# Performance work log

Measured on AMD Instinct MI355X. Metric: run time of the kernel, lower is better.

The kernel has to match this reference:

```python
import jax, jax.numpy as jnp
import numpy as np

TOP_P_THRESHOLD = 1.0 - 0.9  # hardcoded in the original module (ignores self.top_p)

def setup_inputs() -> dict:
    key = jax.random.key(0)
    k1, _ = jax.random.split(key)
    batch, vocab = 128, 128000
    logits = jax.random.normal(k1, (batch, vocab), dtype=jnp.float32) * 3.0
    position_ids = jnp.arange(batch, dtype=jnp.int32)
    return {"logits": logits, "position_ids": position_ids}

def reference(logits, position_ids):
    # Ascending sort along vocab axis (jnp.sort default), matching original.
    sorted_logits = jnp.sort(logits, axis=-1)
    sorted_indices = jnp.argsort(logits, axis=-1)
    # Cumulative probability in ascending-logit order.
    cum_probs = jnp.cumsum(jax.nn.softmax(sorted_logits, axis=-1), axis=-1)
    keep = cum_probs > TOP_P_THRESHOLD
    # Kept sorted values; dropped positions get -inf (the fill_value).
    vals = jnp.where(keep, sorted_logits, -jnp.inf)
    # Scatter back to original vocab positions: mask[..., sorted_indices] = vals
    # is equivalent to gathering vals with the inverse permutation.
    inv_perm = jnp.argsort(sorted_indices, axis=-1)
    mask = jnp.take_along_axis(vals, inv_perm, axis=-1)
    return mask
```

## Files before the change

### kernel.cpp

```cpp
#include <hip/hip_runtime.h>
#include <stdint.h>
#include <math.h>

#define TPB 256
#define CH 16
#define LISTCAP 160
#define FIN_TPB 256
#define FB_TPB 1024
#define FB_TIE 1024
#define S_FIX 4096.0f
#define DROPV (-1.0e30f)

struct SelT { double P; double THR; uint32_t pfx; uint32_t pad; };

__device__ __forceinline__ uint32_t tokey(float f) {
  uint32_t b = __float_as_uint(f);
  return (b & 0x80000000u) ? ~b : (b | 0x80000000u);
}
__device__ __forceinline__ float fromkey(uint32_t k) {
  uint32_t b = (k & 0x80000000u) ? (k ^ 0x80000000u) : ~k;
  return __uint_as_float(b);
}
__device__ __forceinline__ float scrub(float f) {
  uint32_t b = __float_as_uint(f) & 0x7FFFFFFFu;
  if (b >= 0x7F7F0000u) return DROPV;
  return f;
}
__device__ __forceinline__ unsigned long long tofix(float u) {
  return (unsigned long long)(u * S_FIX);
}

__device__ __forceinline__ void wave_selectD(const double* __restrict__ bins, int nb,
                                             int bits, int lane,
                                             double* sP, uint32_t* sPrefix, double THR) {
  const int per = nb >> 6;
  double lsum = 0.0;
  for (int k = 0; k < per; ++k) lsum += bins[lane * per + k];
  double v = lsum;
#pragma unroll
  for (int off = 1; off < 64; off <<= 1) {
    double o = __shfl_up(v, off, 64);
    if (lane >= off) v += o;
  }
  const double excl = v - lsum;
  const double P = *sP;
  int lbin = -1;
  double lP = 0.0;
  double rr = P + excl;
  for (int k = 0; k < per; ++k) {
    double m = bins[lane * per + k];
    double nr = rr + m;
    if (lbin < 0 && nr > THR) { lbin = lane * per + k; lP = rr; }
    rr = nr;
  }
  unsigned long long got = __ballot(lbin >= 0);
  int bsel;
  double Pn;
  if (got) {
    int src = __ffsll(got) - 1;
    bsel = __shfl(lbin, src, 64);
    Pn = __shfl(lP, src, 64);
  } else {
    int hb = -1;
    double pb = P;
    rr = P + excl;
    for (int k = 0; k < per; ++k) {
      double m = bins[lane * per + k];
      if (m > 0.0) { hb = lane * per + k; pb = rr; }
      rr += m;
    }
#pragma unroll
    for (int off = 32; off; off >>= 1) {
      int ob = __shfl_xor(hb, off, 64);
      double opb = __shfl_xor(pb, off, 64);
      if (ob > hb) { hb = ob; pb = opb; }
    }
    bsel = hb < 0 ? (nb - 1) : hb;
    Pn = pb;
  }
  if (lane == 0) {
    *sPrefix = (*sPrefix << bits) | (uint32_t)bsel;
    *sP = Pn;
  }
}

__global__ void zeroK(uint32_t* p, int n) {
  int i = blockIdx.x * blockDim.x + threadIdx.x;
  if (i < n) p[i] = 0u;
}

__global__ __launch_bounds__(TPB) void histZK(const float* __restrict__ x, int V,
                                              unsigned long long* __restrict__ ghist) {
  const int row = blockIdx.y, chunk = blockIdx.x, tid = threadIdx.x;
  const float* rowp = x + (size_t)row * (size_t)V;
  __shared__ unsigned long long h[512 * 4];
  for (int i = tid; i < 2048; i += TPB) h[i] = 0ull;
  __syncthreads();

  const int epc = (((V + CH - 1) / CH) + 3) & ~3;
  const int start = chunk * epc;
  const int end = min(start + epc, V);
  const int vs = start >> 2, ve = end >> 2;
  const int rep = tid & 3;
  auto acc = [&](float4 v) {
    float vv[4] = {v.x, v.y, v.z, v.w};
#pragma unroll
    for (int k = 0; k < 4; ++k) {
      float u = __expf(vv[k]);
      atomicAdd(&h[(((tokey(vv[k]) >> 23) << 2) | rep)], tofix(u));
    }
  };
  for (int i = vs + tid; i < ve; i += 2 * TPB) {
    const int i1 = i + TPB;
    const bool g1 = i1 < ve;
    float4 a = *reinterpret_cast<const float4*>(rowp + 4 * i);
    float4 b;
    if (g1) b = *reinterpret_cast<const float4*>(rowp + 4 * i1);
    acc(a);
    if (g1) acc(b);
  }
  for (int i = (ve << 2) + tid; i < end; i += TPB)
    atomicAdd(&h[(((tokey(rowp[i]) >> 23) << 2) | rep)], tofix(__expf(rowp[i])));
  __syncthreads();
  unsigned long long* gh = ghist + (size_t)row * 512;
  for (int b = tid; b < 512; b += TPB) {
    unsigned long long s = h[4 * b] + h[4 * b + 1] + h[4 * b + 2] + h[4 * b + 3];
    if (s) atomicAdd(&gh[b], s);
  }
}

__global__ __launch_bounds__(64) void sel0K(unsigned long long* __restrict__ ghist,
                                            SelT* __restrict__ sel) {
  const int row = blockIdx.x, lane = threadIdx.x;
  __shared__ double db[512];
  __shared__ double ssP;
  __shared__ uint32_t ssPfx;
  unsigned long long* gh = ghist + (size_t)row * 512;
  double t = 0.0;
  for (int i = lane; i < 512; i += 64) {
    double d = (double)gh[i];
    db[i] = d;
    t += d;
  }
#pragma unroll
  for (int off = 32; off; off >>= 1) t += __shfl_xor(t, off, 64);
  const double THR = (double)0.1f * t;
  if (lane == 0) { ssP = 0.0; ssPfx = 0u; }
  __syncthreads();
  wave_selectD(db, 512, 9, lane, &ssP, &ssPfx, THR);
  __syncthreads();
  if (lane == 0) {
    SelT s;
    s.P = ssP; s.THR = THR; s.pfx = ssPfx; s.pad = 0u;
    sel[row] = s;
  }
  for (int i = lane; i < 512; i += 64) gh[i] = 0ull;
}

__global__ __launch_bounds__(TPB) void outK(const float* __restrict__ x,
                                            float* __restrict__ out, int V,
                                            const SelT* __restrict__ sel,
                                            unsigned long long* __restrict__ ghist) {
  const int row = blockIdx.y, chunk = blockIdx.x, tid = threadIdx.x;
  const float* rowp = x + (size_t)row * (size_t)V;
  float* orow = out + (size_t)row * (size_t)V;
  __shared__ unsigned long long h[512];
  for (int i = tid; i < 512; i += TPB) h[i] = 0ull;
  __syncthreads();
  const uint32_t pfx9 = sel[row].pfx;

  const int epc = (((V + CH - 1) / CH) + 3) & ~3;
  const int start = chunk * epc;
  const int end = min(start + epc, V);
  const int vs = start >> 2, ve = end >> 2;
  auto proc = [&](float4 v, int i) {
    float vv[4] = {v.x, v.y, v.z, v.w};
    float ov[4];
#pragma unroll
    for (int k = 0; k < 4; ++k) {
      uint32_t key = tokey(vv[k]);
      uint32_t top = key >> 23;
      ov[k] = (top > pfx9) ? scrub(vv[k]) : DROPV;
      if (top == pfx9)
        atomicAdd(&h[(key >> 14) & 511u], tofix(__expf(vv[k])));
    }
    *reinterpret_cast<float4*>(orow + 4 * i) = make_float4(ov[0], ov[1], ov[2], ov[3]);
  };
  for (int i = vs + tid; i < ve; i += 2 * TPB) {
    const int i1 = i + TPB;
    const bool g1 = i1 < ve;
    float4 a = *reinterpret_cast<const float4*>(rowp + 4 * i);
    float4 b;
    if (g1) b = *reinterpret_cast<const float4*>(rowp + 4 * i1);
    proc(a, i);
    if (g1) proc(b, i1);
  }
  for (int i = (ve << 2) + tid; i < end; i += TPB) {
    float f = rowp[i];
    uint32_t key = tokey(f);
    uint32_t top = key >> 23;
    orow[i] = (top > pfx9) ? scrub(f) : DROPV;
    if (top == pfx9) atomicAdd(&h[(key >> 14) & 511u], tofix(__expf(f)));
  }
  __syncthreads();
  unsigned long long* gh = ghist + (size_t)row * 512;
  for (int b = tid; b < 512; b += TPB)
    if (h[b]) atomicAdd(&gh[b], h[b]);
}

__global__ __launch_bounds__(64) void sel1K(const unsigned long long* __restrict__ ghist,
                                            SelT* __restrict__ sel) {
  const int row = blockIdx.x, lane = threadIdx.x;
  __shared__ double db[512];
  __shared__ double ssP;
  __shared__ uint32_t ssPfx;
  const unsigned long long* gh = ghist + (size_t)row * 512;
  for (int i = lane; i < 512; i += 64) db[i] = (double)gh[i];
  SelT s = sel[row];
  if (lane == 0) { ssP = s.P; ssPfx = s.pfx; }
  __syncthreads();
  wave_selectD(db, 512, 9, lane, &ssP, &ssPfx, s.THR);
  __syncthreads();
  if (lane == 0) {
    s.P = ssP; s.pfx = ssPfx;
    sel[row] = s;
  }
}

__global__ __launch_bounds__(TPB) void collectK(const float* __restrict__ x,
                                                float* __restrict__ out, int V,
                                                const SelT* __restrict__ sel,
                                                uint2* __restrict__ glist,
                                                uint32_t* __restrict__ gcnt) {
  const int row = blockIdx.y, chunk = blockIdx.x, tid = threadIdx.x;
  const float* rowp = x + (size_t)row * (size_t)V;
  float* orow = out + (size_t)row * (size_t)V;
  const uint32_t pfx18 = sel[row].pfx;
  const uint32_t pfx9 = pfx18 >> 9;
  const uint32_t l1bin = pfx18 & 511u;

  const int epc = (((V + CH - 1) / CH) + 3) & ~3;
  const int start = chunk * epc;
  const int end = min(start + epc, V);
  const int vs = start >> 2, ve = end >> 2;
  auto proc = [&](float f, int idx) {
    uint32_t key = tokey(f);
    if ((key >> 23) == pfx9) {
      uint32_t mid = (key >> 14) & 511u;
      if (mid > l1bin) {
        orow[idx] = scrub(f);
      } else if (mid == l1bin) {
        uint32_t p = atomicAdd(gcnt + row, 1u);
        if (p < LISTCAP) glist[(size_t)row * LISTCAP + p] = make_uint2(key, (uint32_t)idx);
      }
    }
  };
  for (int i = vs + tid; i < ve; i += 2 * TPB) {
    const int i1 = i + TPB;
    const bool g1 = i1 < ve;
    float4 a = *reinterpret_cast<const float4*>(rowp + 4 * i);
    float4 b;
    if (g1) b = *reinterpret_cast<const float4*>(rowp + 4 * i1);
    proc(a.x, 4 * i); proc(a.y, 4 * i + 1); proc(a.z, 4 * i + 2); proc(a.w, 4 * i + 3);
    if (g1) {
      proc(b.x, 4 * i1); proc(b.y, 4 * i1 + 1); proc(b.z, 4 * i1 + 2); proc(b.w, 4 * i1 + 3);
    }
  }
  for (int i = (ve << 2) + tid; i < end; i += TPB) proc(rowp[i], i);
}

__global__ __launch_bounds__(FIN_TPB) void finK(const float* __restrict__ x,
                                                float* __restrict__ out, int V,
                                                const SelT* __restrict__ sel,
                                                const uint2* __restrict__ glist,
                                                const uint32_t* __restrict__ gcnt) {
  const int row = blockIdx.x, tid = threadIdx.x;
  const float* rowp = x + (size_t)row * (size_t)V;
  float* orow = out + (size_t)row * (size_t)V;
  __shared__ uint2 ls[2048];
  __shared__ uint2 srt[2048];
  __shared__ unsigned char keep[2048];
  __shared__ uint32_t scnt;
  const SelT s = sel[row];
  const uint32_t n0 = gcnt[row];
  if (tid == 0) scnt = 0u;
  __syncthreads();
  uint32_t m;
  if (n0 <= LISTCAP) {
    for (uint32_t i = tid; i < n0; i += FIN_TPB)
      ls[i] = glist[(size_t)row * LISTCAP + i];
    m = n0;
    __syncthreads();
  } else {
    const uint32_t pfx18 = s.pfx;
    const int nvec = V >> 2;
    for (int i = tid; i < nvec; i += FIN_TPB) {
      float4 v = *reinterpret_cast<const float4*>(rowp + 4 * i);
      float vv[4] = {v.x, v.y, v.z, v.w};
#pragma unroll
      for (int k = 0; k < 4; ++k) {
        uint32_t key = tokey(vv[k]);
        if ((key >> 14) == pfx18) {
          uint32_t p = atomicAdd(&scnt, 1u);
          if (p < 2048u) ls[p] = make_uint2(key, (uint32_t)(4 * i + k));
        }
      }
    }
    for (int i = (nvec << 2) + tid; i < V; i += FIN_TPB) {
      uint32_t key = tokey(rowp[i]);
      if ((key >> 14) == pfx18) {
        uint32_t p = atomicAdd(&scnt, 1u);
        if (p < 2048u) ls[p] = make_uint2(key, (uint32_t)i);
      }
    }
    __syncthreads();
    m = min(scnt, 2048u);
  }

  for (uint32_t j = tid; j < m; j += FIN_TPB) {
    uint2 kv = ls[j];
    uint32_t r = 0;
    for (uint32_t i = 0; i < m; ++i) {
      uint2 o = ls[i];
      if (o.x < kv.x || (o.x == kv.x && o.y < kv.y)) ++r;
    }
    srt[r] = kv;
  }
  __syncthreads();
  if (tid == 0) {
    double cum = s.P;
    for (uint32_t j = 0; j < m; ++j) {
      cum += (double)__expf(fromkey(srt[j].x)) * (double)S_FIX;
      keep[j] = (cum > s.THR) ? 1 : 0;
    }
  }
  __syncthreads();
  for (uint32_t j = tid; j < m; j += FIN_TPB)
    orow[srt[j].y] = keep[j] ? scrub(fromkey(srt[j].x)) : DROPV;
}

__global__ __launch_bounds__(FB_TPB) void toppK_fb(const float* __restrict__ x,
                                                   float* __restrict__ out, int V) {
  const int row = blockIdx.x;
  const int tid = threadIdx.x;
  const int lane = tid & 63;
  const float* rowp = x + (size_t)row * (size_t)V;
  float* orow = out + (size_t)row * (size_t)V;
  const int nvec = V >> 2;
  const int tail = nvec << 2;

  __shared__ float smass[2048];
  __shared__ double zw[FB_TPB / 64];
  __shared__ double sTHR, sP;
  __shared__ uint32_t sPrefix;
  __shared__ uint32_t sTie[FB_TIE];
  __shared__ uint32_t sTieCnt;
  __shared__ int sD;

  if (tid == 0) { sTieCnt = 0u; sPrefix = 0u; sP = 0.0; sTHR = 0.0; sD = 0; }
  const int shifts[3] = {21, 10, 0};
  const int bitsA[3] = {11, 11, 10};

  for (int L = 0; L < 3; ++L) {
    const int nb = 1 << bitsA[L];
    for (int i = tid; i < nb; i += FB_TPB) smass[i] = 0.f;
    __syncthreads();
    const uint32_t pfx = sPrefix;
    float zloc = 0.f;
    for (int i = tid; i < nvec; i += FB_TPB) {
      float4 v = *reinterpret_cast<const float4*>(rowp + 4 * i);
      float vv[4] = {v.x, v.y, v.z, v.w};
#pragma unroll
      for (int k = 0; k < 4; ++k) {
        uint32_t key = tokey(vv[k]);
        if (L == 0) {
          float u = __expf(vv[k]);
          zloc += u;
          atomicAdd(&smass[key >> 21], u);
        } else if ((key >> (shifts[L] + bitsA[L])) == pfx) {
          atomicAdd(&smass[(key >> shifts[L]) & (uint32_t)(nb - 1)], __expf(vv[k]));
        }
      }
    }
    for (int i = tail + tid; i < V; i += FB_TPB) {
      float f = rowp[i];
      uint32_t key = tokey(f);
      if (L == 0) {
        float u = __expf(f);
        zloc += u;
        atomicAdd(&smass[key >> 21], u);
      } else if ((key >> (shifts[L] + bitsA[L])) == pfx) {
        atomicAdd(&smass[(key >> shifts[L]) & (uint32_t)(nb - 1)], __expf(f));
      }
    }
    if (L == 0) {
      double z = (double)zloc;
#pragma unroll
      for (int off = 32; off; off >>= 1) z += __shfl_down(z, off, 64);
      if (lane == 0) zw[tid >> 6] = z;
    }
    __syncthreads();
    if (L == 0 && tid == 0) {
      double Z = 0.0;
      for (int w = 0; w < FB_TPB / 64; ++w) Z += zw[w];
      sTHR = (double)0.1f * Z;
    }
    __syncthreads();
    if (tid < 64) {
      __shared__ double dtmp[2048];
      for (int i = lane; i < nb; i += 64) dtmp[i] = (double)smass[i];
      wave_selectD(dtmp, nb, bitsA[L], lane, &sP, &sPrefix, sTHR);
    }
    __syncthreads();
  }

  const uint32_t tkey = sPrefix;
  const float tstar = scrub(fromkey(tkey));
  if (tid == 0) {
    double ut = (double)__expf(tstar);
    double dd = floor((sTHR - sP) / ut);
    sD = (dd < 0.0) ? 0 : (dd > 2.0e9 ? 2000000000 : (int)dd);
  }
  __syncthreads();

  for (int i = tid; i < nvec; i += FB_TPB) {
    float4 v = *reinterpret_cast<const float4*>(rowp + 4 * i);
    float vv[4] = {v.x, v.y, v.z, v.w};
    float ov[4];
#pragma unroll
    for (int k = 0; k < 4; ++k) {
      uint32_t key = tokey(vv[k]);
      if (key > tkey) {
        ov[k] = scrub(vv[k]);
      } else {
        ov[k] = DROPV;
        if (key == tkey) {
          uint32_t p = atomicAdd(&sTieCnt, 1u);
          if (p < FB_TIE) sTie[p] = (uint32_t)(4 * i + k);
        }
      }
    }
    *reinterpret_cast<float4*>(orow + 4 * i) = make_float4(ov[0], ov[1], ov[2], ov[3]);
  }
  for (int i = tail + tid; i < V; i += FB_TPB) {
    float f = rowp[i];
    uint32_t key = tokey(f);
    float o = DROPV;
    if (key > tkey) o = scrub(f);
    else if (key == tkey) {
      uint32_t p = atomicAdd(&sTieCnt, 1u);
      if (p < FB_TIE) sTie[p] = (uint32_t)i;
    }
    orow[i] = o;
  }
  __syncthreads();

  uint32_t n = sTieCnt;
  if (n > FB_TIE) n = FB_TIE;
  if (n) {
    if (tid == 0) {
      for (uint32_t i2 = 1; i2 < n; ++i2) {
        uint32_t k2 = sTie[i2];
        int j = (int)i2 - 1;
        while (j >= 0 && sTie[j] > k2) { sTie[j + 1] = sTie[j]; --j; }
        sTie[j + 1] = k2;
      }
      if (sD > (int)n - 1) sD = (int)n - 1;
    }
    __syncthreads();
    const int d = sD;
    for (uint32_t j = tid; j < n; j += FB_TPB)
      orow[sTie[j]] = ((int)j >= d) ? tstar : DROPV;
  }
}

extern "C" void kernel_launch(void* const* d_in, const int* in_sizes, int n_in,
                              void* d_out, int out_size, void* d_ws, size_t ws_size,
                              hipStream_t stream) {
  const float* logits = (const float*)d_in[0];
  const int R = in_sizes[1];
  const int V = in_sizes[0] / R;
  float* out = (float*)d_out;
  (void)out_size; (void)n_in;

  char* ws = (char*)d_ws;
  size_t o = 0;
  auto take = [&](size_t bytes) -> char* {
    char* p = ws + o;
    o = (o + bytes + 7) & ~(size_t)7;
    return p;
  };
  unsigned long long* ghist = (unsigned long long*)take(8ull * R * 512);
  uint32_t* gcnt = (uint32_t*)take(4ull * R);
  const size_t zero_bytes = o;
  SelT* sel = (SelT*)take(sizeof(SelT) * R);
  uint2* glist = (uint2*)take(8ull * R * LISTCAP);
  const size_t need = o;

  if (ws_size < need || (V & 3) != 0) {
    toppK_fb<<<dim3(R), dim3(FB_TPB), 0, stream>>>(logits, out, V);
    return;
  }

  const int zwords = (int)(zero_bytes / 4);
  zeroK<<<dim3((zwords + TPB - 1) / TPB), dim3(TPB), 0, stream>>>((uint32_t*)ws, zwords);

  dim3 grid(CH, R);
  histZK<<<grid, dim3(TPB), 0, stream>>>(logits, V, ghist);
  sel0K<<<dim3(R), dim3(64), 0, stream>>>(ghist, sel);
  outK<<<grid, dim3(TPB), 0, stream>>>(logits, out, V, sel, ghist);
  sel1K<<<dim3(R), dim3(64), 0, stream>>>(ghist, sel);
  collectK<<<grid, dim3(TPB), 0, stream>>>(logits, out, V, sel, glist, gcnt);
  finK<<<dim3(R), dim3(FIN_TPB), 0, stream>>>(logits, out, V, sel, glist, gcnt);
}
```

Measured before the change: 81.67 us.

## Fold per-row selection kernels into consumer kernels via redundant histogram scans

```diff
diff --git a/kernel.cpp b/kernel.cpp
--- a/kernel.cpp
+++ b/kernel.cpp
@@ -4,14 +4,11 @@
 
 #define TPB 256
 #define CH 16
-#define LISTCAP 160
-#define FIN_TPB 256
+#define LISTCAP 192
 #define FB_TPB 1024
 #define FB_TIE 1024
 #define S_FIX 4096.0f
 #define DROPV (-1.0e30f)
-
-struct SelT { double P; double THR; uint32_t pfx; uint32_t pad; };
 
 __device__ __forceinline__ uint32_t tokey(float f) {
   uint32_t b = __float_as_uint(f);
@@ -84,31 +81,58 @@
   }
 }
 
+__device__ __forceinline__ void head_select0(const unsigned long long* __restrict__ gh0,
+                                             double* db, int tid, int lane,
+                                             double* sP, double* sThr, uint32_t* sPfx) {
+  if (tid < 64) {
+    double t = 0.0;
+    for (int i = lane; i < 512; i += 64) {
+      double d = (double)gh0[i];
+      db[i] = d;
+      t += d;
+    }
+#pragma unroll
+    for (int off = 32; off; off >>= 1) t += __shfl_xor(t, off, 64);
+    if (lane == 0) { *sThr = (double)0.1f * t; *sP = 0.0; *sPfx = 0u; }
+  }
+  __syncthreads();
+  if (tid < 64) wave_selectD(db, 512, 9, lane, sP, sPfx, *sThr);
+  __syncthreads();
+}
+
+__device__ __forceinline__ void head_select1(const unsigned long long* __restrict__ gh1,
+                                             double* db, int tid, int lane,
+                                             double* sP, double* sThr, uint32_t* sPfx) {
+  if (tid < 64) {
+    for (int i = lane; i < 256; i += 64) db[i] = (double)gh1[i];
+  }
+  __syncthreads();
+  if (tid < 64) wave_selectD(db, 256, 8, lane, sP, sPfx, *sThr);
+  __syncthreads();
+}
+
 __global__ void zeroK(uint32_t* p, int n) {
   int i = blockIdx.x * blockDim.x + threadIdx.x;
   if (i < n) p[i] = 0u;
 }
 
 __global__ __launch_bounds__(TPB) void histZK(const float* __restrict__ x, int V,
-                                              unsigned long long* __restrict__ ghist) {
+                                              unsigned long long* __restrict__ ghist0) {
   const int row = blockIdx.y, chunk = blockIdx.x, tid = threadIdx.x;
   const float* rowp = x + (size_t)row * (size_t)V;
-  __shared__ unsigned long long h[512 * 4];
+  __shared__ unsigned long long h[2048];
   for (int i = tid; i < 2048; i += TPB) h[i] = 0ull;
   __syncthreads();
 
   const int epc = (((V + CH - 1) / CH) + 3) & ~3;
-  const int start = chunk * epc;
-  const int end = min(start + epc, V);
+  const int start = chunk * epc, end = min(start + epc, V);
   const int vs = start >> 2, ve = end >> 2;
   const int rep = tid & 3;
   auto acc = [&](float4 v) {
     float vv[4] = {v.x, v.y, v.z, v.w};
 #pragma unroll
-    for (int k = 0; k < 4; ++k) {
-      float u = __expf(vv[k]);
-      atomicAdd(&h[(((tokey(vv[k]) >> 23) << 2) | rep)], tofix(u));
-    }
+    for (int k = 0; k < 4; ++k)
+      atomicAdd(&h[(((tokey(vv[k]) >> 23) << 2) | rep)], tofix(__expf(vv[k])));
   };
   for (int i = vs + tid; i < ve; i += 2 * TPB) {
     const int i1 = i + TPB;
@@ -122,56 +146,32 @@
   for (int i = (ve << 2) + tid; i < end; i += TPB)
     atomicAdd(&h[(((tokey(rowp[i]) >> 23) << 2) | rep)], tofix(__expf(rowp[i])));
   __syncthreads();
-  unsigned long long* gh = ghist + (size_t)row * 512;
+  unsigned long long* gh = ghist0 + (size_t)row * 512;
   for (int b = tid; b < 512; b += TPB) {
     unsigned long long s = h[4 * b] + h[4 * b + 1] + h[4 * b + 2] + h[4 * b + 3];
     if (s) atomicAdd(&gh[b], s);
   }
 }
 
-__global__ __launch_bounds__(64) void sel0K(unsigned long long* __restrict__ ghist,
-                                            SelT* __restrict__ sel) {
-  const int row = blockIdx.x, lane = threadIdx.x;
-  __shared__ double db[512];
-  __shared__ double ssP;
-  __shared__ uint32_t ssPfx;
-  unsigned long long* gh = ghist + (size_t)row * 512;
-  double t = 0.0;
-  for (int i = lane; i < 512; i += 64) {
-    double d = (double)gh[i];
-    db[i] = d;
-    t += d;
-  }
-#pragma unroll
-  for (int off = 32; off; off >>= 1) t += __shfl_xor(t, off, 64);
-  const double THR = (double)0.1f * t;
-  if (lane == 0) { ssP = 0.0; ssPfx = 0u; }
-  __syncthreads();
-  wave_selectD(db, 512, 9, lane, &ssP, &ssPfx, THR);
-  __syncthreads();
-  if (lane == 0) {
-    SelT s;
-    s.P = ssP; s.THR = THR; s.pfx = ssPfx; s.pad = 0u;
-    sel[row] = s;
-  }
-  for (int i = lane; i < 512; i += 64) gh[i] = 0ull;
-}
-
-__global__ __launch_bounds__(TPB) void outK(const float* __restrict__ x,
-                                            float* __restrict__ out, int V,
-                                            const SelT* __restrict__ sel,
-                                            unsigned long long* __restrict__ ghist) {
-  const int row = blockIdx.y, chunk = blockIdx.x, tid = threadIdx.x;
+__global__ __launch_bounds__(TPB) void outSelK(const float* __restrict__ x,
+                                               float* __restrict__ out, int V,
+                                               const unsigned long long* __restrict__ ghist0,
+                                               unsigned long long* __restrict__ ghist1) {
+  const int row = blockIdx.y, chunk = blockIdx.x, tid = threadIdx.x, lane = tid & 63;
   const float* rowp = x + (size_t)row * (size_t)V;
   float* orow = out + (size_t)row * (size_t)V;
-  __shared__ unsigned long long h[512];
-  for (int i = tid; i < 512; i += TPB) h[i] = 0ull;
-  __syncthreads();
-  const uint32_t pfx9 = sel[row].pfx;
+  __shared__ double db[512];
+  __shared__ unsigned long long h[256];
+  __shared__ double sP, sThr;
+  __shared__ uint32_t sPfx;
+
+  head_select0(ghist0 + (size_t)row * 512, db, tid, lane, &sP, &sThr, &sPfx);
+  const uint32_t pfx9 = sPfx;
+  for (int i = tid; i < 256; i += TPB) h[i] = 0ull;
+  __syncthreads();
 
   const int epc = (((V + CH - 1) / CH) + 3) & ~3;
-  const int start = chunk * epc;
-  const int end = min(start + epc, V);
+  const int start = chunk * epc, end = min(start + epc, V);
   const int vs = start >> 2, ve = end >> 2;
   auto proc = [&](float4 v, int i) {
     float vv[4] = {v.x, v.y, v.z, v.w};
@@ -181,8 +181,7 @@
       uint32_t key = tokey(vv[k]);
       uint32_t top = key >> 23;
       ov[k] = (top > pfx9) ? scrub(vv[k]) : DROPV;
-      if (top == pfx9)
-        atomicAdd(&h[(key >> 14) & 511u], tofix(__expf(vv[k])));
+      if (top == pfx9) atomicAdd(&h[(key >> 15) & 255u], tofix(__expf(vv[k])));
     }
     *reinterpret_cast<float4*>(orow + 4 * i) = make_float4(ov[0], ov[1], ov[2], ov[3]);
   };
@@ -197,56 +196,42 @@
   }
   for (int i = (ve << 2) + tid; i < end; i += TPB) {
     float f = rowp[i];
-    uint32_t key = tokey(f);
-    uint32_t top = key >> 23;
+    uint32_t key = tokey(f), top = key >> 23;
     orow[i] = (top > pfx9) ? scrub(f) : DROPV;
-    if (top == pfx9) atomicAdd(&h[(key >> 14) & 511u], tofix(__expf(f)));
-  }
-  __syncthreads();
-  unsigned long long* gh = ghist + (size_t)row * 512;
-  for (int b = tid; b < 512; b += TPB)
-    if (h[b]) atomicAdd(&gh[b], h[b]);
-}
-
-__global__ __launch_bounds__(64) void sel1K(const unsigned long long* __restrict__ ghist,
-                                            SelT* __restrict__ sel) {
-  const int row = blockIdx.x, lane = threadIdx.x;
-  __shared__ double db[512];
-  __shared__ double ssP;
-  __shared__ uint32_t ssPfx;
-  const unsigned long long* gh = ghist + (size_t)row * 512;
-  for (int i = lane; i < 512; i += 64) db[i] = (double)gh[i];
-  SelT s = sel[row];
-  if (lane == 0) { ssP = s.P; ssPfx = s.pfx; }
-  __syncthreads();
-  wave_selectD(db, 512, 9, lane, &ssP, &ssPfx, s.THR);
-  __syncthreads();
-  if (lane == 0) {
-    s.P = ssP; s.pfx = ssPfx;
-    sel[row] = s;
-  }
-}
-
-__global__ __launch_bounds__(TPB) void collectK(const float* __restrict__ x,
-                                                float* __restrict__ out, int V,
-                                                const SelT* __restrict__ sel,
-                                                uint2* __restrict__ glist,
-                                                uint32_t* __restrict__ gcnt) {
-  const int row = blockIdx.y, chunk = blockIdx.x, tid = threadIdx.x;
+    if (top == pfx9) atomicAdd(&h[(key >> 15) & 255u], tofix(__expf(f)));
+  }
+  __syncthreads();
+  unsigned long long* gh1 = ghist1 + (size_t)row * 256;
+  for (int b = tid; b < 256; b += TPB)
+    if (h[b]) atomicAdd(&gh1[b], h[b]);
+}
+
+__global__ __launch_bounds__(TPB) void colSelK(const float* __restrict__ x,
+                                               float* __restrict__ out, int V,
+                                               const unsigned long long* __restrict__ ghist0,
+                                               const unsigned long long* __restrict__ ghist1,
+                                               uint2* __restrict__ glist,
+                                               uint32_t* __restrict__ gcnt) {
+  const int row = blockIdx.y, chunk = blockIdx.x, tid = threadIdx.x, lane = tid & 63;
   const float* rowp = x + (size_t)row * (size_t)V;
   float* orow = out + (size_t)row * (size_t)V;
-  const uint32_t pfx18 = sel[row].pfx;
-  const uint32_t pfx9 = pfx18 >> 9;
-  const uint32_t l1bin = pfx18 & 511u;
+  __shared__ double db[512];
+  __shared__ double sP, sThr;
+  __shared__ uint32_t sPfx;
+
+  head_select0(ghist0 + (size_t)row * 512, db, tid, lane, &sP, &sThr, &sPfx);
+  head_select1(ghist1 + (size_t)row * 256, db, tid, lane, &sP, &sThr, &sPfx);
+  const uint32_t pfx17 = sPfx;
+  const uint32_t pfx9 = pfx17 >> 8;
+  const uint32_t l1bin = pfx17 & 255u;
 
   const int epc = (((V + CH - 1) / CH) + 3) & ~3;
-  const int start = chunk * epc;
-  const int end = min(start + epc, V);
+  const int start = chunk * epc, end = min(start + epc, V);
   const int vs = start >> 2, ve = end >> 2;
   auto proc = [&](float f, int idx) {
     uint32_t key = tokey(f);
     if ((key >> 23) == pfx9) {
-      uint32_t mid = (key >> 14) & 511u;
+      uint32_t mid = (key >> 15) & 255u;
       if (mid > l1bin) {
         orow[idx] = scrub(f);
       } else if (mid == l1bin) {
@@ -254,6 +239,9 @@
         if (p < LISTCAP) glist[(size_t)row * LISTCAP + p] = make_uint2(key, (uint32_t)idx);
       }
     }
+  };
+  auto proc4 = [&](float4 v, int i) {
+    proc(v.x, 4 * i); proc(v.y, 4 * i + 1); proc(v.z, 4 * i + 2); proc(v.w, 4 * i + 3);
   };
   for (int i = vs + tid; i < ve; i += 2 * TPB) {
     const int i1 = i + TPB;
@@ -261,54 +249,59 @@
     float4 a = *reinterpret_cast<const float4*>(rowp + 4 * i);
     float4 b;
     if (g1) b = *reinterpret_cast<const float4*>(rowp + 4 * i1);
-    proc(a.x, 4 * i); proc(a.y, 4 * i + 1); proc(a.z, 4 * i + 2); proc(a.w, 4 * i + 3);
-    if (g1) {
-      proc(b.x, 4 * i1); proc(b.y, 4 * i1 + 1); proc(b.z, 4 * i1 + 2); proc(b.w, 4 * i1 + 3);
-    }
+    proc4(a, i);
+    if (g1) proc4(b, i1);
   }
   for (int i = (ve << 2) + tid; i < end; i += TPB) proc(rowp[i], i);
 }
 
-__global__ __launch_bounds__(FIN_TPB) void finK(const float* __restrict__ x,
-                                                float* __restrict__ out, int V,
-                                                const SelT* __restrict__ sel,
-                                                const uint2* __restrict__ glist,
-                                                const uint32_t* __restrict__ gcnt) {
-  const int row = blockIdx.x, tid = threadIdx.x;
+__global__ __launch_bounds__(TPB) void finSelK(const float* __restrict__ x,
+                                               float* __restrict__ out, int V,
+                                               const unsigned long long* __restrict__ ghist0,
+                                               const unsigned long long* __restrict__ ghist1,
+                                               const uint2* __restrict__ glist,
+                                               const uint32_t* __restrict__ gcnt) {
+  const int row = blockIdx.x, tid = threadIdx.x, lane = tid & 63;
   const float* rowp = x + (size_t)row * (size_t)V;
   float* orow = out + (size_t)row * (size_t)V;
+  __shared__ double db[512];
+  __shared__ double sP, sThr;
+  __shared__ uint32_t sPfx;
   __shared__ uint2 ls[2048];
   __shared__ uint2 srt[2048];
   __shared__ unsigned char keep[2048];
   __shared__ uint32_t scnt;
-  const SelT s = sel[row];
+
+  head_select0(ghist0 + (size_t)row * 512, db, tid, lane, &sP, &sThr, &sPfx);
+  head_select1(ghist1 + (size_t)row * 256, db, tid, lane, &sP, &sThr, &sPfx);
+  const uint32_t pfx17 = sPfx;
+  const double P = sP, THR = sThr;
+
   const uint32_t n0 = gcnt[row];
   if (tid == 0) scnt = 0u;
   __syncthreads();
   uint32_t m;
   if (n0 <= LISTCAP) {
-    for (uint32_t i = tid; i < n0; i += FIN_TPB)
-      ls[i] = glist[(size_t)row * LISTCAP + i];
+    for (uint32_t i = tid; i < n0; i += TPB) ls[i] = glist[(size_t)row * LISTCAP + i];
     m = n0;
     __syncthreads();
   } else {
-    const uint32_t pfx18 = s.pfx;
     const int nvec = V >> 2;
-    for (int i = tid; i < nvec; i += FIN_TPB) {
+    for (int i = tid; i < nvec; i += TPB) {
       float4 v = *reinterpret_cast<const float4*>(rowp + 4 * i);
       float vv[4] = {v.x, v.y, v.z, v.w};
 #pragma unroll
       for (int k = 0; k < 4; ++k) {
         uint32_t key = tokey(vv[k]);
-        if ((key >> 14) == pfx18) {
+        if ((key >> 15) == pfx17) {
           uint32_t p = atomicAdd(&scnt, 1u);
           if (p < 2048u) ls[p] = make_uint2(key, (uint32_t)(4 * i + k));
         }
       }
     }
-    for (int i = (nvec << 2) + tid; i < V; i += FIN_TPB) {
+    for (int i = (nvec << 2) + tid; i < V; i += TPB) {
       uint32_t key = tokey(rowp[i]);
-      if ((key >> 14) == pfx18) {
+      if ((key >> 15) == pfx17) {
         uint32_t p = atomicAdd(&scnt, 1u);
         if (p < 2048u) ls[p] = make_uint2(key, (uint32_t)i);
       }
@@ -317,7 +310,7 @@
     m = min(scnt, 2048u);
   }
 
-  for (uint32_t j = tid; j < m; j += FIN_TPB) {
+  for (uint32_t j = tid; j < m; j += TPB) {
     uint2 kv = ls[j];
     uint32_t r = 0;
     for (uint32_t i = 0; i < m; ++i) {
@@ -328,14 +321,14 @@
   }
   __syncthreads();
   if (tid == 0) {
-    double cum = s.P;
+    double cum = P;
     for (uint32_t j = 0; j < m; ++j) {
       cum += (double)__expf(fromkey(srt[j].x)) * (double)S_FIX;
-      keep[j] = (cum > s.THR) ? 1 : 0;
-    }
-  }
-  __syncthreads();
-  for (uint32_t j = tid; j < m; j += FIN_TPB)
+      keep[j] = (cum > THR) ? 1 : 0;
+    }
+  }
+  __syncthreads();
+  for (uint32_t j = tid; j < m; j += TPB)
     orow[srt[j].y] = keep[j] ? scrub(fromkey(srt[j].x)) : DROPV;
 }
 
@@ -490,10 +483,10 @@
     o = (o + bytes + 7) & ~(size_t)7;
     return p;
   };
-  unsigned long long* ghist = (unsigned long long*)take(8ull * R * 512);
+  unsigned long long* ghist0 = (unsigned long long*)take(8ull * R * 512);
+  unsigned long long* ghist1 = (unsigned long long*)take(8ull * R * 256);
   uint32_t* gcnt = (uint32_t*)take(4ull * R);
   const size_t zero_bytes = o;
-  SelT* sel = (SelT*)take(sizeof(SelT) * R);
   uint2* glist = (uint2*)take(8ull * R * LISTCAP);
   const size_t need = o;
 
@@ -506,10 +499,8 @@
   zeroK<<<dim3((zwords + TPB - 1) / TPB), dim3(TPB), 0, stream>>>((uint32_t*)ws, zwords);
 
   dim3 grid(CH, R);
-  histZK<<<grid, dim3(TPB), 0, stream>>>(logits, V, ghist);
-  sel0K<<<dim3(R), dim3(64), 0, stream>>>(ghist, sel);
-  outK<<<grid, dim3(TPB), 0, stream>>>(logits, out, V, sel, ghist);
-  sel1K<<<dim3(R), dim3(64), 0, stream>>>(ghist, sel);
-  collectK<<<grid, dim3(TPB), 0, stream>>>(logits, out, V, sel, glist, gcnt);
-  finK<<<dim3(R), dim3(FIN_TPB), 0, stream>>>(logits, out, V, sel, glist, gcnt);
-}
+  histZK<<<grid, dim3(TPB), 0, stream>>>(logits, V, ghist0);
+  outSelK<<<grid, dim3(TPB), 0, stream>>>(logits, out, V, ghist0, ghist1);
+  colSelK<<<grid, dim3(TPB), 0, stream>>>(logits, out, V, ghist0, ghist1, glist, gcnt);
+  finSelK<<<dim3(R), dim3(TPB), 0, stream>>>(logits, out, V, ghist0, ghist1, glist, gcnt);
+}
```

Result: slower. 97.73 us (+19.7%).
